# Performance work log

Measured on AMD Instinct MI355X. Metric: run time of the kernel, lower is better.

Reference implementation:

```python
import jax, jax.numpy as jnp
import numpy as np
from jax import lax


def setup_inputs() -> dict:
    key = jax.random.key(0)
    ks = jax.random.split(key, 6)
    B, L, D, H, K = 32, 256, 16, 64, 5
    T = L - K + 1            # 252
    S = (T // 2) * H         # 8064
    return {
        "x": jax.random.normal(ks[0], (B, L, D), dtype=jnp.float32),
        "conv_w": jax.random.normal(ks[1], (D, H, K), dtype=jnp.float32) * 0.1,
        "conv_b": jax.random.normal(ks[2], (D, H), dtype=jnp.float32) * 0.1,
        "deconv_w": jax.random.normal(ks[3], (D, H, K), dtype=jnp.float32) * 0.1,
        "deconv_b": jax.random.normal(ks[4], (D,), dtype=jnp.float32) * 0.1,
        "W_attn": jax.random.normal(ks[5], (S, S), dtype=jnp.float32) * 0.01,
    }


def reference(x, conv_w, conv_b, deconv_w, deconv_b, W_attn):
    B, L, D = x.shape
    _, H, K = conv_w.shape
    T = L - K + 1
    P = T // 2
    S = P * H

    xt = jnp.transpose(x, (0, 2, 1))  # [B, D, L]
    # per-channel Conv1d(1->H) as one grouped conv: kernel [D*H, 1, K], groups=D
    y = lax.conv_general_dilated(
        xt, conv_w.reshape(D * H, 1, K), (1,), "VALID",
        dimension_numbers=("NCH", "OIH", "NCH"), feature_group_count=D,
    ) + conv_b.reshape(1, D * H, 1)
    y = jax.nn.relu(y)  # [B, D*H, T]

    # per-channel ConvTranspose1d(H->1) == full conv with flipped kernel, groups=D
    recon = lax.conv_general_dilated(
        y, deconv_w[..., ::-1], (1,), [(K - 1, K - 1)],
        dimension_numbers=("NCH", "OIH", "NCH"), feature_group_count=D,
    ) + deconv_b.reshape(1, D, 1)  # [B, D, L]

    # AvgPool1d(kernel=2, stride=2) then flatten(H, P) per channel
    pooled = y.reshape(B, D, H, P, 2).mean(axis=-1)  # [B, D, H, P]
    flat = pooled.reshape(B, D, S)                   # [B, D, S]

    main = flat[:, 0]        # [B, S]
    aux = flat[:, 1:]        # [B, D-1, S]

    # 'general' score: main . (aux @ W^T)  ==  (main @ W) . aux
    m = main @ W_attn                              # [B, S]
    scores = jnp.einsum("bt,bdt->bd", m, aux)      # [B, D-1]
    attn = jax.nn.softmax(scores, axis=-1)         # [B, D-1]
    weighted = jnp.einsum("bd,bds->bs", attn, aux)  # [B, S]

    out = jnp.concatenate([main[:, None, :], weighted[:, None, :]], axis=2)  # [B,1,2S]
    return out, attn[:, None, :], recon
```

## Files before the change

kernel.cpp:

```cpp
#include <hip/hip_runtime.h>
#include <math.h>

#define BB 32
#define LL 256
#define DD 16
#define HH 64
#define KK 5
#define TT 252
#define PP 126
#define SS 8064
#define NCHUNK 12
#define CHUNK 672
#define NKT 21
#define NSB 8
#define SLICE 1008

typedef __attribute__((ext_vector_type(8))) short bf16x8;
typedef __attribute__((ext_vector_type(4))) float f32x4;

__device__ __forceinline__ unsigned short f2bf(float f) {
  unsigned int u = __float_as_uint(f);
  u += 0x7FFFu + ((u >> 16) & 1u);
  return (unsigned short)(u >> 16);
}
__device__ __forceinline__ float bf2f(unsigned short h) {
  return __uint_as_float(((unsigned int)h) << 16);
}

__global__ __launch_bounds__(256) void k12_conv_recon(
    const float* __restrict__ x, const float* __restrict__ cw,
    const float* __restrict__ cb, const float* __restrict__ dw,
    const float* __restrict__ db, float* __restrict__ flat,
    unsigned short* __restrict__ mainH, unsigned short* __restrict__ mainL,
    float* __restrict__ recon) {
  __shared__ float ylds[HH * TT];
  __shared__ float xs[LL];
  __shared__ float cws[HH * KK];
  __shared__ float dws[HH * KK];
  __shared__ float cbs[HH];

  int bd = blockIdx.x;
  int b = bd / DD, d = bd % DD;
  int tid = threadIdx.x;

  {
    float4 xv = *(const float4*)(x + ((size_t)b * LL + tid) * DD + (d & ~3));
    int dl = d & 3;
    float v = (dl == 0) ? xv.x : (dl == 1) ? xv.y : (dl == 2) ? xv.z : xv.w;
    xs[tid] = v;
  }
  for (int i = tid; i < HH * KK; i += 256) {
    cws[i] = cw[(size_t)d * HH * KK + i];
    dws[i] = dw[(size_t)d * HH * KK + i];
  }
  if (tid < HH) cbs[tid] = cb[d * HH + tid];
  __syncthreads();

  {
    int h = tid >> 2, a = tid & 3;
    int t0 = a * 63;
    float w0 = cws[h * KK + 0], w1 = cws[h * KK + 1], w2 = cws[h * KK + 2],
          w3 = cws[h * KK + 3], w4 = cws[h * KK + 4];
    float bias = cbs[h];
    float x0 = xs[t0], x1 = xs[t0 + 1], x2 = xs[t0 + 2], x3 = xs[t0 + 3],
          x4 = xs[t0 + 4];
    float* yrow = ylds + h * TT + t0;
    #pragma unroll 7
    for (int t = 0; t < 63; ++t) {
      float yv = fmaf(w4, x4, fmaf(w3, x3, fmaf(w2, x2, fmaf(w1, x1, fmaf(w0, x0, bias)))));
      yrow[t] = fmaxf(yv, 0.f);
      x0 = x1; x1 = x2; x2 = x3; x3 = x4;
      if (t < 62) x4 = xs[t0 + t + 5];
    }
  }
  __syncthreads();

  for (int i = tid; i < HH * PP; i += 256) {
    int h = i / PP, p = i - h * PP;
    float pooled = 0.5f * (ylds[h * TT + 2 * p] + ylds[h * TT + 2 * p + 1]);
    flat[(size_t)bd * SS + i] = pooled;
    if (d == 0) {
      unsigned short hb = f2bf(pooled);
      mainH[(size_t)b * SS + i] = hb;
      mainL[(size_t)b * SS + i] = f2bf(pooled - bf2f(hb));
    }
  }

  {
    int l = tid;
    float acc = db[d];
    for (int h = 0; h < HH; ++h) {
      const float* yl = ylds + h * TT;
      #pragma unroll
      for (int j = 0; j < KK; ++j) {
        int t = l - j;
        if (t >= 0 && t < TT) acc = fmaf(yl[t], dws[h * KK + j], acc);
      }
    }
    recon[(size_t)bd * LL + l] = acc;
  }
}

#define BARRIER_NODRAIN() do {                                        \
    asm volatile("s_waitcnt lgkmcnt(0)" ::: "memory");                \
    __builtin_amdgcn_s_barrier();                                     \
  } while (0)

__global__ __launch_bounds__(256) void k3_mfma(
    const float* __restrict__ W, const unsigned short* __restrict__ mainH,
    const unsigned short* __restrict__ mainL, float* __restrict__ partial) {
  __shared__ unsigned short AH[2][1024];
  __shared__ unsigned short AL[2][1024];
  __shared__ unsigned short BH[2][4096];

  int tid = threadIdx.x;
  int chunk = blockIdx.y;
  int s0 = chunk * CHUNK;
  int cbase = blockIdx.x * 128;

  int lane = tid & 63;
  int wv = tid >> 6;
  int mr = wv & 1;
  int ctb = (wv >> 1) * 4;

  f32x4 c0 = {0.f, 0.f, 0.f, 0.f};
  f32x4 c1 = {0.f, 0.f, 0.f, 0.f};
  f32x4 c2 = {0.f, 0.f, 0.f, 0.f};
  f32x4 c3 = {0.f, 0.f, 0.f, 0.f};

  int sc2 = (tid & 63) * 2;
  int sg = tid >> 6;
  const float* wbase = W + (size_t)(s0 + sg * 8) * SS + cbase + sc2;

  int ab = tid >> 2, aq = tid & 3;
  size_t abase = (size_t)ab * SS + (size_t)(s0 + aq * 8);

  int aoff  = (lane >> 4) * 256 + ((lane & 15) + 16 * mr) * 8;
  int boff0 = (lane >> 4) * 1024 + (ctb * 16 + (lane & 15)) * 8;

  float2 e0, e1, e2, e3, e4, e5, e6, e7;
  float2 o0, o1, o2, o3, o4, o5, o6, o7;
  bf16x8 aEH, aEL, aOH, aOL;

#define LOADW(R0,R1,R2,R3,R4,R5,R6,R7, KT) {                          \
    const float* p_ = wbase + (size_t)(KT) * 32 * SS;                 \
    R0 = *(const float2*)(p_);                                        \
    R1 = *(const float2*)(p_ + (size_t)SS);                           \
    R2 = *(const float2*)(p_ + 2 * (size_t)SS);                       \
    R3 = *(const float2*)(p_ + 3 * (size_t)SS);                       \
    R4 = *(const float2*)(p_ + 4 * (size_t)SS);                       \
    R5 = *(const float2*)(p_ + 5 * (size_t)SS);                       \
    R6 = *(const float2*)(p_ + 6 * (size_t)SS);                       \
    R7 = *(const float2*)(p_ + 7 * (size_t)SS); }

#define LOADA(RH, RL, KT) if (tid < 128) {                            \
    RH = *(const bf16x8*)(mainH + abase + (KT) * 32);                 \
    RL = *(const bf16x8*)(mainL + abase + (KT) * 32); }

#define CVT1(F, J) {                                                  \
    h0[J] = (short)f2bf(F.x);                                         \
    h1[J] = (short)f2bf(F.y); }

#define CVTW(R0,R1,R2,R3,R4,R5,R6,R7, BUF) {                          \
    bf16x8 h0, h1;                                                    \
    CVT1(R0, 0) CVT1(R1, 1) CVT1(R2, 2) CVT1(R3, 3)                   \
    CVT1(R4, 4) CVT1(R5, 5) CVT1(R6, 6) CVT1(R7, 7)                   \
    *(bf16x8*)&BH[BUF][sg * 1024 + sc2 * 8]     = h0;                 \
    *(bf16x8*)&BH[BUF][sg * 1024 + sc2 * 8 + 8] = h1; }

#define WRITEA(RH, RL, BUF) if (tid < 128) {                          \
    *(bf16x8*)&AH[BUF][aq * 256 + ab * 8] = RH;                       \
    *(bf16x8*)&AL[BUF][aq * 256 + ab * 8] = RL; }

#define DOMFMA(BUF) {                                                 \
    bf16x8 ah  = *(const bf16x8*)&AH[BUF][aoff];                      \
    bf16x8 al  = *(const bf16x8*)&AL[BUF][aoff];                      \
    bf16x8 bh0 = *(const bf16x8*)&BH[BUF][boff0];                     \
    bf16x8 bh1 = *(const bf16x8*)&BH[BUF][boff0 + 128];               \
    bf16x8 bh2 = *(const bf16x8*)&BH[BUF][boff0 + 256];               \
    bf16x8 bh3 = *(const bf16x8*)&BH[BUF][boff0 + 384];               \
    c0 = __builtin_amdgcn_mfma_f32_16x16x32_bf16(ah, bh0, c0, 0, 0, 0); \
    c0 = __builtin_amdgcn_mfma_f32_16x16x32_bf16(al, bh0, c0, 0, 0, 0); \
    c1 = __builtin_amdgcn_mfma_f32_16x16x32_bf16(ah, bh1, c1, 0, 0, 0); \
    c1 = __builtin_amdgcn_mfma_f32_16x16x32_bf16(al, bh1, c1, 0, 0, 0); \
    c2 = __builtin_amdgcn_mfma_f32_16x16x32_bf16(ah, bh2, c2, 0, 0, 0); \
    c2 = __builtin_amdgcn_mfma_f32_16x16x32_bf16(al, bh2, c2, 0, 0, 0); \
    c3 = __builtin_amdgcn_mfma_f32_16x16x32_bf16(ah, bh3, c3, 0, 0, 0); \
    c3 = __builtin_amdgcn_mfma_f32_16x16x32_bf16(al, bh3, c3, 0, 0, 0); }

  LOADW(e0,e1,e2,e3,e4,e5,e6,e7, 0) LOADA(aEH, aEL, 0)
  CVTW(e0,e1,e2,e3,e4,e5,e6,e7, 0) WRITEA(aEH, aEL, 0)
  LOADW(o0,o1,o2,o3,o4,o5,o6,o7, 1) LOADA(aOH, aOL, 1)
  __syncthreads();

  #pragma unroll 1
  for (int kt = 0; kt < NKT - 1; kt += 2) {
    LOADW(e0,e1,e2,e3,e4,e5,e6,e7, kt + 2) LOADA(aEH, aEL, kt + 2)
    DOMFMA(0)
    CVTW(o0,o1,o2,o3,o4,o5,o6,o7, 1) WRITEA(aOH, aOL, 1)
    BARRIER_NODRAIN();
    if (kt + 3 < NKT) {
      LOADW(o0,o1,o2,o3,o4,o5,o6,o7, kt + 3) LOADA(aOH, aOL, kt + 3)
    }
    DOMFMA(1)
    CVTW(e0,e1,e2,e3,e4,e5,e6,e7, 0) WRITEA(aEH, aEL, 0)
    BARRIER_NODRAIN();
  }
  DOMFMA(0)

  int row0 = mr * 16 + (lane >> 4) * 4;
  int col0 = cbase + ctb * 16 + (lane & 15);
  float* pp = partial + ((size_t)chunk * BB + row0) * SS + col0;
  #pragma unroll
  for (int r = 0; r < 4; ++r) pp[(size_t)r * SS]      = c0[r];
  #pragma unroll
  for (int r = 0; r < 4; ++r) pp[(size_t)r * SS + 16] = c1[r];
  #pragma unroll
  for (int r = 0; r < 4; ++r) pp[(size_t)r * SS + 32] = c2[r];
  #pragma unroll
  for (int r = 0; r < 4; ++r) pp[(size_t)r * SS + 48] = c3[r];
#undef LOADW
#undef LOADA
#undef CVT1
#undef CVTW
#undef WRITEA
#undef DOMFMA
}

__global__ __launch_bounds__(256) void k4_scores(
    const float* __restrict__ partial, const float* __restrict__ flat,
    float* __restrict__ pscores) {
  int sb = blockIdx.x;
  int b = blockIdx.y;
  int tid = threadIdx.x;

  float acc[15];
  #pragma unroll
  for (int dd = 0; dd < 15; ++dd) acc[dd] = 0.f;

  const float* pb = partial + (size_t)b * SS;
  const float* fb = flat + (size_t)b * DD * SS;

  for (int s = sb * SLICE + tid; s < (sb + 1) * SLICE; s += 256) {
    float mv = 0.f;
    #pragma unroll
    for (int c = 0; c < NCHUNK; ++c)
      mv += pb[(size_t)c * (BB * SS) + s];
    #pragma unroll
    for (int dd = 0; dd < 15; ++dd)
      acc[dd] = fmaf(mv, fb[(size_t)(1 + dd) * SS + s], acc[dd]);
  }

  #pragma unroll
  for (int dd = 0; dd < 15; ++dd) {
    float v = acc[dd];
    #pragma unroll
    for (int o = 32; o; o >>= 1) v += __shfl_xor(v, o);
    acc[dd] = v;
  }
  __shared__ float red[4][15];
  if ((tid & 63) == 0) {
    int w = tid >> 6;
    #pragma unroll
    for (int dd = 0; dd < 15; ++dd) red[w][dd] = acc[dd];
  }
  __syncthreads();
  if (tid < 15)
    pscores[(size_t)sb * (BB * 15) + b * 15 + tid] =
        red[0][tid] + red[1][tid] + red[2][tid] + red[3][tid];
}

__global__ __launch_bounds__(256) void k6_out(
    const float* __restrict__ flat, const float* __restrict__ pscores,
    float* __restrict__ out, float* __restrict__ attn_out) {
  int b = blockIdx.y;
  int s = blockIdx.x * 256 + threadIdx.x;

#define SUMS(DD_) ({ float t_ = 0.f;                                   \
    _Pragma("unroll")                                                  \
    for (int sb_ = 0; sb_ < NSB; ++sb_)                                \
      t_ += pscores[(size_t)sb_ * (BB * 15) + b * 15 + (DD_)];         \
    t_; })
  float v0 = SUMS(0),  v1 = SUMS(1),  v2 = SUMS(2),  v3 = SUMS(3),
        v4 = SUMS(4),  v5 = SUMS(5),  v6 = SUMS(6),  v7 = SUMS(7),
        v8 = SUMS(8),  v9 = SUMS(9),  v10 = SUMS(10), v11 = SUMS(11),
        v12 = SUMS(12), v13 = SUMS(13), v14 = SUMS(14);
#undef SUMS
  float mx = -INFINITY;
  mx = fmaxf(mx, v0);  mx = fmaxf(mx, v1);  mx = fmaxf(mx, v2);
  mx = fmaxf(mx, v3);  mx = fmaxf(mx, v4);  mx = fmaxf(mx, v5);
  mx = fmaxf(mx, v6);  mx = fmaxf(mx, v7);  mx = fmaxf(mx, v8);
  mx = fmaxf(mx, v9);  mx = fmaxf(mx, v10); mx = fmaxf(mx, v11);
  mx = fmaxf(mx, v12); mx = fmaxf(mx, v13); mx = fmaxf(mx, v14);
  float a0 = expf(v0 - mx), a1 = expf(v1 - mx), a2 = expf(v2 - mx),
        a3 = expf(v3 - mx), a4 = expf(v4 - mx), a5 = expf(v5 - mx),
        a6 = expf(v6 - mx), a7 = expf(v7 - mx), a8 = expf(v8 - mx),
        a9 = expf(v9 - mx), a10 = expf(v10 - mx), a11 = expf(v11 - mx),
        a12 = expf(v12 - mx), a13 = expf(v13 - mx), a14 = expf(v14 - mx);
  float sum = a0 + a1 + a2 + a3 + a4 + a5 + a6 + a7 + a8 + a9 + a10 + a11 +
              a12 + a13 + a14;
  float inv = 1.f / sum;

  if (blockIdx.x == 0 && threadIdx.x < 15) {
    float v = 0.f;
    #pragma unroll
    for (int sb_ = 0; sb_ < NSB; ++sb_)
      v += pscores[(size_t)sb_ * (BB * 15) + b * 15 + threadIdx.x];
    attn_out[b * 15 + threadIdx.x] = expf(v - mx) * inv;
  }

  if (s >= SS) return;
  const float* fb = flat + (size_t)b * DD * SS;
  out[(size_t)b * 2 * SS + s] = fb[s];
  float w = 0.f;
  w = fmaf(a0 * inv,  fb[(size_t)1 * SS + s], w);
  w = fmaf(a1 * inv,  fb[(size_t)2 * SS + s], w);
  w = fmaf(a2 * inv,  fb[(size_t)3 * SS + s], w);
  w = fmaf(a3 * inv,  fb[(size_t)4 * SS + s], w);
  w = fmaf(a4 * inv,  fb[(size_t)5 * SS + s], w);
  w = fmaf(a5 * inv,  fb[(size_t)6 * SS + s], w);
  w = fmaf(a6 * inv,  fb[(size_t)7 * SS + s], w);
  w = fmaf(a7 * inv,  fb[(size_t)8 * SS + s], w);
  w = fmaf(a8 * inv,  fb[(size_t)9 * SS + s], w);
  w = fmaf(a9 * inv,  fb[(size_t)10 * SS + s], w);
  w = fmaf(a10 * inv, fb[(size_t)11 * SS + s], w);
  w = fmaf(a11 * inv, fb[(size_t)12 * SS + s], w);
  w = fmaf(a12 * inv, fb[(size_t)13 * SS + s], w);
  w = fmaf(a13 * inv, fb[(size_t)14 * SS + s], w);
  w = fmaf(a14 * inv, fb[(size_t)15 * SS + s], w);
  out[(size_t)b * 2 * SS + SS + s] = w;
}

extern "C" void kernel_launch(void* const* d_in, const int* in_sizes, int n_in,
                              void* d_out, int out_size, void* d_ws, size_t ws_size,
                              hipStream_t stream) {
  const float* x        = (const float*)d_in[0];
  const float* conv_w   = (const float*)d_in[1];
  const float* conv_b   = (const float*)d_in[2];
  const float* deconv_w = (const float*)d_in[3];
  const float* deconv_b = (const float*)d_in[4];
  const float* W_attn   = (const float*)d_in[5];
  float* out = (float*)d_out;

  const size_t ATTN_OFF  = (size_t)BB * 2 * SS;
  const size_t RECON_OFF = ATTN_OFF + (size_t)BB * 15;

  float* ws      = (float*)d_ws;
  float* partial = ws;
  float* flat    = partial + (size_t)NCHUNK * BB * SS;
  unsigned short* mainH = (unsigned short*)(flat + (size_t)BB * DD * SS);
  unsigned short* mainL = mainH + (size_t)BB * SS;
  float* pscores = (float*)(mainL + (size_t)BB * SS);

  k12_conv_recon<<<dim3(BB * DD), dim3(256), 0, stream>>>(
      x, conv_w, conv_b, deconv_w, deconv_b, flat, mainH, mainL, out + RECON_OFF);

  k3_mfma<<<dim3(SS / 128, NCHUNK), dim3(256), 0, stream>>>(
      W_attn, mainH, mainL, partial);

  k4_scores<<<dim3(NSB, BB), dim3(256), 0, stream>>>(partial, flat, pscores);

  k6_out<<<dim3((SS + 255) / 256, BB), dim3(256), 0, stream>>>(
      flat, pscores, out, out + ATTN_OFF);
}
```

Measured before the change: 89.96 us.

## Double k-step depth per stage in W GEMV-MFMA kernel and use 14 chunks

```diff
diff --git a/kernel.cpp b/kernel.cpp
--- a/kernel.cpp
+++ b/kernel.cpp
@@ -9,9 +9,9 @@
 #define TT 252
 #define PP 126
 #define SS 8064
-#define NCHUNK 12
-#define CHUNK 672
-#define NKT 21
+#define NCHUNK 14
+#define CHUNK 576
+#define NKT 9
 #define NSB 8
 #define SLICE 1008
 
@@ -109,9 +109,9 @@
 __global__ __launch_bounds__(256) void k3_mfma(
     const float* __restrict__ W, const unsigned short* __restrict__ mainH,
     const unsigned short* __restrict__ mainL, float* __restrict__ partial) {
-  __shared__ unsigned short AH[2][1024];
-  __shared__ unsigned short AL[2][1024];
-  __shared__ unsigned short BH[2][4096];
+  __shared__ unsigned short AH[2][2048];
+  __shared__ unsigned short AL[2][2048];
+  __shared__ unsigned short BH[2][8192];
 
   int tid = threadIdx.x;
   int chunk = blockIdx.y;
@@ -132,78 +132,108 @@
   int sg = tid >> 6;
   const float* wbase = W + (size_t)(s0 + sg * 8) * SS + cbase + sc2;
 
-  int ab = tid >> 2, aq = tid & 3;
-  size_t abase = (size_t)ab * SS + (size_t)(s0 + aq * 8);
-
-  int aoff  = (lane >> 4) * 256 + ((lane & 15) + 16 * mr) * 8;
+  int ab8 = tid >> 3, aq8 = tid & 7;
+  size_t abase = (size_t)ab8 * SS + (size_t)(s0 + aq8 * 8);
+
+  int aoff0 = ((lane >> 4)) * 256 + ((lane & 15) + 16 * mr) * 8;
+  int aoff1 = aoff0 + 4 * 256;
   int boff0 = (lane >> 4) * 1024 + (ctb * 16 + (lane & 15)) * 8;
 
-  float2 e0, e1, e2, e3, e4, e5, e6, e7;
-  float2 o0, o1, o2, o3, o4, o5, o6, o7;
+  float2 e0, e1, e2, e3, e4, e5, e6, e7, e8, e9, e10, e11, e12, e13, e14, e15;
+  float2 o0, o1, o2, o3, o4, o5, o6, o7, o8, o9, o10, o11, o12, o13, o14, o15;
   bf16x8 aEH, aEL, aOH, aOL;
 
-#define LOADW(R0,R1,R2,R3,R4,R5,R6,R7, KT) {                          \
-    const float* p_ = wbase + (size_t)(KT) * 32 * SS;                 \
-    R0 = *(const float2*)(p_);                                        \
-    R1 = *(const float2*)(p_ + (size_t)SS);                           \
-    R2 = *(const float2*)(p_ + 2 * (size_t)SS);                       \
-    R3 = *(const float2*)(p_ + 3 * (size_t)SS);                       \
-    R4 = *(const float2*)(p_ + 4 * (size_t)SS);                       \
-    R5 = *(const float2*)(p_ + 5 * (size_t)SS);                       \
-    R6 = *(const float2*)(p_ + 6 * (size_t)SS);                       \
-    R7 = *(const float2*)(p_ + 7 * (size_t)SS); }
-
-#define LOADA(RH, RL, KT) if (tid < 128) {                            \
-    RH = *(const bf16x8*)(mainH + abase + (KT) * 32);                 \
-    RL = *(const bf16x8*)(mainL + abase + (KT) * 32); }
-
-#define CVT1(F, J) {                                                  \
-    h0[J] = (short)f2bf(F.x);                                         \
-    h1[J] = (short)f2bf(F.y); }
-
-#define CVTW(R0,R1,R2,R3,R4,R5,R6,R7, BUF) {                          \
-    bf16x8 h0, h1;                                                    \
-    CVT1(R0, 0) CVT1(R1, 1) CVT1(R2, 2) CVT1(R3, 3)                   \
-    CVT1(R4, 4) CVT1(R5, 5) CVT1(R6, 6) CVT1(R7, 7)                   \
-    *(bf16x8*)&BH[BUF][sg * 1024 + sc2 * 8]     = h0;                 \
-    *(bf16x8*)&BH[BUF][sg * 1024 + sc2 * 8 + 8] = h1; }
-
-#define WRITEA(RH, RL, BUF) if (tid < 128) {                          \
-    *(bf16x8*)&AH[BUF][aq * 256 + ab * 8] = RH;                       \
-    *(bf16x8*)&AL[BUF][aq * 256 + ab * 8] = RL; }
+#define LOADW(P, KT) {                                                \
+    const float* p_ = wbase + (size_t)(KT) * 64 * SS;                 \
+    P##0 = *(const float2*)(p_);                                      \
+    P##1 = *(const float2*)(p_ + (size_t)SS);                         \
+    P##2 = *(const float2*)(p_ + 2 * (size_t)SS);                     \
+    P##3 = *(const float2*)(p_ + 3 * (size_t)SS);                     \
+    P##4 = *(const float2*)(p_ + 4 * (size_t)SS);                     \
+    P##5 = *(const float2*)(p_ + 5 * (size_t)SS);                     \
+    P##6 = *(const float2*)(p_ + 6 * (size_t)SS);                     \
+    P##7 = *(const float2*)(p_ + 7 * (size_t)SS);                     \
+    const float* q_ = p_ + 32 * (size_t)SS;                           \
+    P##8  = *(const float2*)(q_);                                     \
+    P##9  = *(const float2*)(q_ + (size_t)SS);                        \
+    P##10 = *(const float2*)(q_ + 2 * (size_t)SS);                    \
+    P##11 = *(const float2*)(q_ + 3 * (size_t)SS);                    \
+    P##12 = *(const float2*)(q_ + 4 * (size_t)SS);                    \
+    P##13 = *(const float2*)(q_ + 5 * (size_t)SS);                    \
+    P##14 = *(const float2*)(q_ + 6 * (size_t)SS);                    \
+    P##15 = *(const float2*)(q_ + 7 * (size_t)SS); }
+
+#define LOADA(RH, RL, KT) {                                           \
+    RH = *(const bf16x8*)(mainH + abase + (size_t)(KT) * 64);         \
+    RL = *(const bf16x8*)(mainL + abase + (size_t)(KT) * 64); }
+
+#define CVT1(H0, H1, F, J) {                                          \
+    H0[J] = (short)f2bf(F.x);                                         \
+    H1[J] = (short)f2bf(F.y); }
+
+#define CVTW(P, BUF) {                                                \
+    bf16x8 h0, h1, h2, h3;                                            \
+    CVT1(h0, h1, P##0, 0) CVT1(h0, h1, P##1, 1)                       \
+    CVT1(h0, h1, P##2, 2) CVT1(h0, h1, P##3, 3)                       \
+    CVT1(h0, h1, P##4, 4) CVT1(h0, h1, P##5, 5)                       \
+    CVT1(h0, h1, P##6, 6) CVT1(h0, h1, P##7, 7)                       \
+    CVT1(h2, h3, P##8, 0)  CVT1(h2, h3, P##9, 1)                      \
+    CVT1(h2, h3, P##10, 2) CVT1(h2, h3, P##11, 3)                     \
+    CVT1(h2, h3, P##12, 4) CVT1(h2, h3, P##13, 5)                     \
+    CVT1(h2, h3, P##14, 6) CVT1(h2, h3, P##15, 7)                     \
+    *(bf16x8*)&BH[BUF][sg * 1024 + sc2 * 8]            = h0;          \
+    *(bf16x8*)&BH[BUF][sg * 1024 + sc2 * 8 + 8]        = h1;          \
+    *(bf16x8*)&BH[BUF][(sg + 4) * 1024 + sc2 * 8]      = h2;          \
+    *(bf16x8*)&BH[BUF][(sg + 4) * 1024 + sc2 * 8 + 8]  = h3; }
+
+#define WRITEA(RH, RL, BUF) {                                         \
+    *(bf16x8*)&AH[BUF][aq8 * 256 + ab8 * 8] = RH;                     \
+    *(bf16x8*)&AL[BUF][aq8 * 256 + ab8 * 8] = RL; }
 
 #define DOMFMA(BUF) {                                                 \
-    bf16x8 ah  = *(const bf16x8*)&AH[BUF][aoff];                      \
-    bf16x8 al  = *(const bf16x8*)&AL[BUF][aoff];                      \
-    bf16x8 bh0 = *(const bf16x8*)&BH[BUF][boff0];                     \
-    bf16x8 bh1 = *(const bf16x8*)&BH[BUF][boff0 + 128];               \
-    bf16x8 bh2 = *(const bf16x8*)&BH[BUF][boff0 + 256];               \
-    bf16x8 bh3 = *(const bf16x8*)&BH[BUF][boff0 + 384];               \
-    c0 = __builtin_amdgcn_mfma_f32_16x16x32_bf16(ah, bh0, c0, 0, 0, 0); \
-    c0 = __builtin_amdgcn_mfma_f32_16x16x32_bf16(al, bh0, c0, 0, 0, 0); \
-    c1 = __builtin_amdgcn_mfma_f32_16x16x32_bf16(ah, bh1, c1, 0, 0, 0); \
-    c1 = __builtin_amdgcn_mfma_f32_16x16x32_bf16(al, bh1, c1, 0, 0, 0); \
-    c2 = __builtin_amdgcn_mfma_f32_16x16x32_bf16(ah, bh2, c2, 0, 0, 0); \
-    c2 = __builtin_amdgcn_mfma_f32_16x16x32_bf16(al, bh2, c2, 0, 0, 0); \
-    c3 = __builtin_amdgcn_mfma_f32_16x16x32_bf16(ah, bh3, c3, 0, 0, 0); \
-    c3 = __builtin_amdgcn_mfma_f32_16x16x32_bf16(al, bh3, c3, 0, 0, 0); }
-
-  LOADW(e0,e1,e2,e3,e4,e5,e6,e7, 0) LOADA(aEH, aEL, 0)
-  CVTW(e0,e1,e2,e3,e4,e5,e6,e7, 0) WRITEA(aEH, aEL, 0)
-  LOADW(o0,o1,o2,o3,o4,o5,o6,o7, 1) LOADA(aOH, aOL, 1)
+    bf16x8 ah0 = *(const bf16x8*)&AH[BUF][aoff0];                     \
+    bf16x8 al0 = *(const bf16x8*)&AL[BUF][aoff0];                     \
+    bf16x8 ah1 = *(const bf16x8*)&AH[BUF][aoff1];                     \
+    bf16x8 al1 = *(const bf16x8*)&AL[BUF][aoff1];                     \
+    bf16x8 b00 = *(const bf16x8*)&BH[BUF][boff0];                     \
+    bf16x8 b01 = *(const bf16x8*)&BH[BUF][boff0 + 4096];              \
+    bf16x8 b10 = *(const bf16x8*)&BH[BUF][boff0 + 128];               \
+    bf16x8 b11 = *(const bf16x8*)&BH[BUF][boff0 + 128 + 4096];        \
+    bf16x8 b20 = *(const bf16x8*)&BH[BUF][boff0 + 256];               \
+    bf16x8 b21 = *(const bf16x8*)&BH[BUF][boff0 + 256 + 4096];        \
+    bf16x8 b30 = *(const bf16x8*)&BH[BUF][boff0 + 384];               \
+    bf16x8 b31 = *(const bf16x8*)&BH[BUF][boff0 + 384 + 4096];        \
+    c0 = __builtin_amdgcn_mfma_f32_16x16x32_bf16(ah0, b00, c0, 0, 0, 0); \
+    c0 = __builtin_amdgcn_mfma_f32_16x16x32_bf16(al0, b00, c0, 0, 0, 0); \
+    c0 = __builtin_amdgcn_mfma_f32_16x16x32_bf16(ah1, b01, c0, 0, 0, 0); \
+    c0 = __builtin_amdgcn_mfma_f32_16x16x32_bf16(al1, b01, c0, 0, 0, 0); \
+    c1 = __builtin_amdgcn_mfma_f32_16x16x32_bf16(ah0, b10, c1, 0, 0, 0); \
+    c1 = __builtin_amdgcn_mfma_f32_16x16x32_bf16(al0, b10, c1, 0, 0, 0); \
+    c1 = __builtin_amdgcn_mfma_f32_16x16x32_bf16(ah1, b11, c1, 0, 0, 0); \
+    c1 = __builtin_amdgcn_mfma_f32_16x16x32_bf16(al1, b11, c1, 0, 0, 0); \
+    c2 = __builtin_amdgcn_mfma_f32_16x16x32_bf16(ah0, b20, c2, 0, 0, 0); \
+    c2 = __builtin_amdgcn_mfma_f32_16x16x32_bf16(al0, b20, c2, 0, 0, 0); \
+    c2 = __builtin_amdgcn_mfma_f32_16x16x32_bf16(ah1, b21, c2, 0, 0, 0); \
+    c2 = __builtin_amdgcn_mfma_f32_16x16x32_bf16(al1, b21, c2, 0, 0, 0); \
+    c3 = __builtin_amdgcn_mfma_f32_16x16x32_bf16(ah0, b30, c3, 0, 0, 0); \
+    c3 = __builtin_amdgcn_mfma_f32_16x16x32_bf16(al0, b30, c3, 0, 0, 0); \
+    c3 = __builtin_amdgcn_mfma_f32_16x16x32_bf16(ah1, b31, c3, 0, 0, 0); \
+    c3 = __builtin_amdgcn_mfma_f32_16x16x32_bf16(al1, b31, c3, 0, 0, 0); }
+
+  LOADW(e, 0) LOADA(aEH, aEL, 0)
+  CVTW(e, 0) WRITEA(aEH, aEL, 0)
+  LOADW(o, 1) LOADA(aOH, aOL, 1)
   __syncthreads();
 
   #pragma unroll 1
   for (int kt = 0; kt < NKT - 1; kt += 2) {
-    LOADW(e0,e1,e2,e3,e4,e5,e6,e7, kt + 2) LOADA(aEH, aEL, kt + 2)
+    LOADW(e, kt + 2) LOADA(aEH, aEL, kt + 2)
     DOMFMA(0)
-    CVTW(o0,o1,o2,o3,o4,o5,o6,o7, 1) WRITEA(aOH, aOL, 1)
+    CVTW(o, 1) WRITEA(aOH, aOL, 1)
     BARRIER_NODRAIN();
-    if (kt + 3 < NKT) {
-      LOADW(o0,o1,o2,o3,o4,o5,o6,o7, kt + 3) LOADA(aOH, aOL, kt + 3)
-    }
+    if (kt + 3 < NKT) { LOADW(o, kt + 3) LOADA(aOH, aOL, kt + 3) }
     DOMFMA(1)
-    CVTW(e0,e1,e2,e3,e4,e5,e6,e7, 0) WRITEA(aEH, aEL, 0)
+    CVTW(e, 0) WRITEA(aEH, aEL, 0)
     BARRIER_NODRAIN();
   }
   DOMFMA(0)
```

Measured after the change: 92.17 us. 1.02x slower.

## Feed W directly from registers into 32x32x16 MFMA, skipping LDS staging

Applied to the files above, without the earlier changes.

```diff
diff --git a/kernel.cpp b/kernel.cpp
--- a/kernel.cpp
+++ b/kernel.cpp
@@ -9,14 +9,15 @@
 #define TT 252
 #define PP 126
 #define SS 8064
-#define NCHUNK 12
-#define CHUNK 672
-#define NKT 21
+#define NCHUNK 14
+#define CHUNK 576
+#define NSTEP 36
+#define NG 6
 #define NSB 8
 #define SLICE 1008
 
 typedef __attribute__((ext_vector_type(8))) short bf16x8;
-typedef __attribute__((ext_vector_type(4))) float f32x4;
+typedef __attribute__((ext_vector_type(16))) float f32x16;
 
 __device__ __forceinline__ unsigned short f2bf(float f) {
   unsigned int u = __float_as_uint(f);
@@ -109,122 +110,99 @@
 __global__ __launch_bounds__(256) void k3_mfma(
     const float* __restrict__ W, const unsigned short* __restrict__ mainH,
     const unsigned short* __restrict__ mainL, float* __restrict__ partial) {
-  __shared__ unsigned short AH[2][1024];
-  __shared__ unsigned short AL[2][1024];
-  __shared__ unsigned short BH[2][4096];
+  __shared__ unsigned short AH[2][3072];
+  __shared__ unsigned short AL[2][3072];
 
   int tid = threadIdx.x;
+  int lane = tid & 63;
+  int wv = tid >> 6;
   int chunk = blockIdx.y;
   int s0 = chunk * CHUNK;
-  int cbase = blockIdx.x * 128;
-
-  int lane = tid & 63;
-  int wv = tid >> 6;
-  int mr = wv & 1;
-  int ctb = (wv >> 1) * 4;
-
-  f32x4 c0 = {0.f, 0.f, 0.f, 0.f};
-  f32x4 c1 = {0.f, 0.f, 0.f, 0.f};
-  f32x4 c2 = {0.f, 0.f, 0.f, 0.f};
-  f32x4 c3 = {0.f, 0.f, 0.f, 0.f};
-
-  int sc2 = (tid & 63) * 2;
-  int sg = tid >> 6;
-  const float* wbase = W + (size_t)(s0 + sg * 8) * SS + cbase + sc2;
-
-  int ab = tid >> 2, aq = tid & 3;
-  size_t abase = (size_t)ab * SS + (size_t)(s0 + aq * 8);
-
-  int aoff  = (lane >> 4) * 256 + ((lane & 15) + 16 * mr) * 8;
-  int boff0 = (lane >> 4) * 1024 + (ctb * 16 + (lane & 15)) * 8;
-
-  float2 e0, e1, e2, e3, e4, e5, e6, e7;
-  float2 o0, o1, o2, o3, o4, o5, o6, o7;
-  bf16x8 aEH, aEL, aOH, aOL;
-
-#define LOADW(R0,R1,R2,R3,R4,R5,R6,R7, KT) {                          \
-    const float* p_ = wbase + (size_t)(KT) * 32 * SS;                 \
-    R0 = *(const float2*)(p_);                                        \
-    R1 = *(const float2*)(p_ + (size_t)SS);                           \
-    R2 = *(const float2*)(p_ + 2 * (size_t)SS);                       \
-    R3 = *(const float2*)(p_ + 3 * (size_t)SS);                       \
-    R4 = *(const float2*)(p_ + 4 * (size_t)SS);                       \
-    R5 = *(const float2*)(p_ + 5 * (size_t)SS);                       \
-    R6 = *(const float2*)(p_ + 6 * (size_t)SS);                       \
-    R7 = *(const float2*)(p_ + 7 * (size_t)SS); }
-
-#define LOADA(RH, RL, KT) if (tid < 128) {                            \
-    RH = *(const bf16x8*)(mainH + abase + (KT) * 32);                 \
-    RL = *(const bf16x8*)(mainL + abase + (KT) * 32); }
-
-#define CVT1(F, J) {                                                  \
-    h0[J] = (short)f2bf(F.x);                                         \
-    h1[J] = (short)f2bf(F.y); }
-
-#define CVTW(R0,R1,R2,R3,R4,R5,R6,R7, BUF) {                          \
-    bf16x8 h0, h1;                                                    \
-    CVT1(R0, 0) CVT1(R1, 1) CVT1(R2, 2) CVT1(R3, 3)                   \
-    CVT1(R4, 4) CVT1(R5, 5) CVT1(R6, 6) CVT1(R7, 7)                   \
-    *(bf16x8*)&BH[BUF][sg * 1024 + sc2 * 8]     = h0;                 \
-    *(bf16x8*)&BH[BUF][sg * 1024 + sc2 * 8 + 8] = h1; }
-
-#define WRITEA(RH, RL, BUF) if (tid < 128) {                          \
-    *(bf16x8*)&AH[BUF][aq * 256 + ab * 8] = RH;                       \
-    *(bf16x8*)&AL[BUF][aq * 256 + ab * 8] = RL; }
-
-#define DOMFMA(BUF) {                                                 \
-    bf16x8 ah  = *(const bf16x8*)&AH[BUF][aoff];                      \
-    bf16x8 al  = *(const bf16x8*)&AL[BUF][aoff];                      \
-    bf16x8 bh0 = *(const bf16x8*)&BH[BUF][boff0];                     \
-    bf16x8 bh1 = *(const bf16x8*)&BH[BUF][boff0 + 128];               \
-    bf16x8 bh2 = *(const bf16x8*)&BH[BUF][boff0 + 256];               \
-    bf16x8 bh3 = *(const bf16x8*)&BH[BUF][boff0 + 384];               \
-    c0 = __builtin_amdgcn_mfma_f32_16x16x32_bf16(ah, bh0, c0, 0, 0, 0); \
-    c0 = __builtin_amdgcn_mfma_f32_16x16x32_bf16(al, bh0, c0, 0, 0, 0); \
-    c1 = __builtin_amdgcn_mfma_f32_16x16x32_bf16(ah, bh1, c1, 0, 0, 0); \
-    c1 = __builtin_amdgcn_mfma_f32_16x16x32_bf16(al, bh1, c1, 0, 0, 0); \
-    c2 = __builtin_amdgcn_mfma_f32_16x16x32_bf16(ah, bh2, c2, 0, 0, 0); \
-    c2 = __builtin_amdgcn_mfma_f32_16x16x32_bf16(al, bh2, c2, 0, 0, 0); \
-    c3 = __builtin_amdgcn_mfma_f32_16x16x32_bf16(ah, bh3, c3, 0, 0, 0); \
-    c3 = __builtin_amdgcn_mfma_f32_16x16x32_bf16(al, bh3, c3, 0, 0, 0); }
-
-  LOADW(e0,e1,e2,e3,e4,e5,e6,e7, 0) LOADA(aEH, aEL, 0)
-  CVTW(e0,e1,e2,e3,e4,e5,e6,e7, 0) WRITEA(aEH, aEL, 0)
-  LOADW(o0,o1,o2,o3,o4,o5,o6,o7, 1) LOADA(aOH, aOL, 1)
+  int n0 = blockIdx.x * 128 + wv * 32;
+  int colq = lane & 31;
+  int koct = lane >> 5;
+
+  const float* wb = W + (size_t)(s0 + koct * 8) * SS + n0 + colq;
+
+  f32x16 acc;
+  #pragma unroll
+  for (int r = 0; r < 16; ++r) acc[r] = 0.f;
+
+  float wA0, wA1, wA2, wA3, wA4, wA5, wA6, wA7;
+  float wB0, wB1, wB2, wB3, wB4, wB5, wB6, wB7;
+  float wC0, wC1, wC2, wC3, wC4, wC5, wC6, wC7;
+  bf16x8 aH1, aL1, aH2, aL2;
+
+  int arow = tid & 31, aoct = tid >> 5;
+
+#define LOADW(P, T) if ((T) < NSTEP) {                                \
+    const float* p_ = wb + (size_t)(T) * 16 * SS;                     \
+    P##0 = p_[0];                P##1 = p_[(size_t)SS];               \
+    P##2 = p_[2 * (size_t)SS];   P##3 = p_[3 * (size_t)SS];           \
+    P##4 = p_[4 * (size_t)SS];   P##5 = p_[5 * (size_t)SS];           \
+    P##6 = p_[6 * (size_t)SS];   P##7 = p_[7 * (size_t)SS]; }
+
+#define LOADA(G) {                                                    \
+    size_t kb_ = (size_t)s0 + (size_t)(G) * 96;                       \
+    aH1 = *(const bf16x8*)(mainH + (size_t)arow * SS + kb_ + aoct * 8); \
+    aL1 = *(const bf16x8*)(mainL + (size_t)arow * SS + kb_ + aoct * 8); \
+    if (tid < 128) {                                                  \
+      aH2 = *(const bf16x8*)(mainH + (size_t)arow * SS + kb_ + (aoct + 8) * 8); \
+      aL2 = *(const bf16x8*)(mainL + (size_t)arow * SS + kb_ + (aoct + 8) * 8); \
+    } }
+
+#define WRITEA(BUF) {                                                 \
+    *(bf16x8*)&AH[BUF][tid * 8] = aH1;                                \
+    *(bf16x8*)&AL[BUF][tid * 8] = aL1;                                \
+    if (tid < 128) {                                                  \
+      *(bf16x8*)&AH[BUF][(tid + 256) * 8] = aH2;                      \
+      *(bf16x8*)&AL[BUF][(tid + 256) * 8] = aL2;                      \
+    } }
+
+#define CONSUME(P, KS, BUF) {                                         \
+    bf16x8 bh;                                                        \
+    bh[0] = (short)f2bf(P##0); bh[1] = (short)f2bf(P##1);             \
+    bh[2] = (short)f2bf(P##2); bh[3] = (short)f2bf(P##3);             \
+    bh[4] = (short)f2bf(P##4); bh[5] = (short)f2bf(P##5);             \
+    bh[6] = (short)f2bf(P##6); bh[7] = (short)f2bf(P##7);             \
+    int aoff_ = ((KS) * 2 + koct) * 256 + colq * 8;                   \
+    bf16x8 ah = *(const bf16x8*)&AH[BUF][aoff_];                      \
+    bf16x8 al = *(const bf16x8*)&AL[BUF][aoff_];                      \
+    acc = __builtin_amdgcn_mfma_f32_32x32x16_bf16(ah, bh, acc, 0, 0, 0); \
+    acc = __builtin_amdgcn_mfma_f32_32x32x16_bf16(al, bh, acc, 0, 0, 0); }
+
+  LOADA(0)
+  WRITEA(0)
+  LOADA(1)
+  LOADW(wA, 0)
+  LOADW(wB, 1)
   __syncthreads();
 
   #pragma unroll 1
-  for (int kt = 0; kt < NKT - 1; kt += 2) {
-    LOADW(e0,e1,e2,e3,e4,e5,e6,e7, kt + 2) LOADA(aEH, aEL, kt + 2)
-    DOMFMA(0)
-    CVTW(o0,o1,o2,o3,o4,o5,o6,o7, 1) WRITEA(aOH, aOL, 1)
-    BARRIER_NODRAIN();
-    if (kt + 3 < NKT) {
-      LOADW(o0,o1,o2,o3,o4,o5,o6,o7, kt + 3) LOADA(aOH, aOL, kt + 3)
-    }
-    DOMFMA(1)
-    CVTW(e0,e1,e2,e3,e4,e5,e6,e7, 0) WRITEA(aEH, aEL, 0)
-    BARRIER_NODRAIN();
-  }
-  DOMFMA(0)
-
-  int row0 = mr * 16 + (lane >> 4) * 4;
-  int col0 = cbase + ctb * 16 + (lane & 15);
-  float* pp = partial + ((size_t)chunk * BB + row0) * SS + col0;
+  for (int g = 0; g < NG; ++g) {
+    int base = g * 6;
+    int buf = g & 1;
+    LOADW(wC, base + 2)  CONSUME(wA, 0, buf)
+    LOADW(wA, base + 3)  CONSUME(wB, 1, buf)
+    LOADW(wB, base + 4)  CONSUME(wC, 2, buf)
+    LOADW(wC, base + 5)  CONSUME(wA, 3, buf)
+    LOADW(wA, base + 6)  CONSUME(wB, 4, buf)
+    LOADW(wB, base + 7)  CONSUME(wC, 5, buf)
+    if (g + 1 < NG) { WRITEA(buf ^ 1) }
+    if (g + 2 < NG) { LOADA(g + 2) }
+    if (g + 1 < NG) BARRIER_NODRAIN();
+  }
+
+  float* pp = partial + (size_t)chunk * BB * SS + n0 + colq;
   #pragma unroll
-  for (int r = 0; r < 4; ++r) pp[(size_t)r * SS]      = c0[r];
-  #pragma unroll
-  for (int r = 0; r < 4; ++r) pp[(size_t)r * SS + 16] = c1[r];
-  #pragma unroll
-  for (int r = 0; r < 4; ++r) pp[(size_t)r * SS + 32] = c2[r];
-  #pragma unroll
-  for (int r = 0; r < 4; ++r) pp[(size_t)r * SS + 48] = c3[r];
+  for (int r = 0; r < 16; ++r) {
+    int row = (r & 3) + 8 * (r >> 2) + 4 * koct;
+    pp[(size_t)row * SS] = acc[r];
+  }
 #undef LOADW
 #undef LOADA
-#undef CVT1
-#undef CVTW
 #undef WRITEA
-#undef DOMFMA
+#undef CONSUME
 }
 
 __global__ __launch_bounds__(256) void k4_scores(
```

Result: slower. 96.24 us (+7.0%).
